# Performance work log

Measured on AMD Instinct MI355X. Metric: run time of the kernel, lower is better.

Reference implementation:

```python
import jax, jax.numpy as jnp
import numpy as np

NORMALIZED_LENGTH = 1.0
LOSS_WEIGHTS = (0.25, 1.0)
EPS = 1e-12  # matches torch F.normalize eps


def setup_inputs() -> dict:
    key = jax.random.key(0)
    k1, k2 = jax.random.split(key)
    x = jax.random.normal(k1, (16, 128, 64, 64), dtype=jnp.float32)
    codebook = jax.random.normal(k2, (1024, 128), dtype=jnp.float32)
    return {"x": x, "codebook": codebook}


def _forward(x, codebook):
    # --- VQCodebook.forward: normalize x along channel dim (dim=1) ---
    # NOTE: the torch source's codebook renormalization uses non-in-place
    # .div/.mul whose results are discarded, so the codebook is unchanged.
    if NORMALIZED_LENGTH > 0:
        nrm = jnp.linalg.norm(x, axis=1, keepdims=True)  # [B,1,H,W]
        x = NORMALIZED_LENGTH * x / jnp.maximum(nrm, EPS)

    B, C, H, W = x.shape
    z = jnp.transpose(x, (0, 2, 3, 1)).reshape(-1, C)  # [N, C], N = B*H*W

    # Pairwise squared L2 distances via ||z||^2 - 2 z c^T + ||c||^2.
    # argmin of squared distance == argmin of distance.
    z2 = jnp.sum(z * z, axis=1, keepdims=True)             # [N, 1]
    c2 = jnp.sum(codebook * codebook, axis=1)              # [K]
    d2 = z2 - 2.0 * jnp.einsum('nc,kc->nk', z, codebook) + c2[None, :]  # [N, K]
    idx = jnp.argmin(d2, axis=1)                           # [N]

    q = codebook[idx]                                      # [N, C]
    q = q.reshape(B, H, W, C).transpose(0, 3, 1, 2)        # [B, C, H, W]

    lw0, lw1 = LOSS_WEIGHTS
    diff_codebook = jax.lax.stop_gradient(x) - q
    diff_commit = x - jax.lax.stop_gradient(q)
    loss0 = lw0 * jnp.mean(jnp.linalg.norm(diff_codebook, axis=1))
    loss1 = lw1 * jnp.mean(jnp.linalg.norm(diff_commit, axis=1))
    return q, loss0, loss1


def reference(x, codebook):
    return _forward(x, codebook)
```

## Files before the change

kernel.cpp:

```cpp
#include <hip/hip_runtime.h>
#include <math.h>

#define K_CODES 1024
#define C_DIM   128
#define HW      4096
#define CHW     (C_DIM*HW)
#define N_POS   65536
#define Q_ELEMS 8388608

#define WS_S    0
#define WS_C2   256
#define WS_IDX  8192


typedef __attribute__((ext_vector_type(8))) short short8;
typedef __attribute__((ext_vector_type(4))) float f32x4;

__device__ __forceinline__ unsigned short f2bf(float f) {
    unsigned u = __float_as_uint(f);
    u += 0x7FFFu + ((u >> 16) & 1u);
    return (unsigned short)(u >> 16);
}

__device__ __forceinline__ void gll16(const void* g, void* l) {
    __builtin_amdgcn_global_load_lds(
        (const __attribute__((address_space(1))) void*)g,
        (__attribute__((address_space(3))) void*)l, 16, 0, 0);
}

__global__ void prep_kernel(const float* __restrict__ cb, float* __restrict__ ws,
                            unsigned short* __restrict__ cbbf) {
    __shared__ __align__(16) unsigned short srow[128];
    int k = blockIdx.x;
    int l = threadIdx.x;
    if (k == 0 && l == 0) *(float*)((char*)ws + WS_S) = 0.f;
    float v1 = cb[k * C_DIM + l];
    float v2 = cb[k * C_DIM + 64 + l];
    int c1 = l, c2 = 64 + l;
    srow[(((c1 >> 3) ^ (k & 7)) << 3) | (c1 & 7)] = f2bf(v1);
    srow[(((c2 >> 3) ^ (k & 7)) << 3) | (c2 & 7)] = f2bf(v2);
    float ss = v1 * v1 + v2 * v2;
    #pragma unroll
    for (int off = 32; off > 0; off >>= 1) ss += __shfl_down(ss, off);
    if (l == 0) ((float*)((char*)ws + WS_C2))[k] = ss;
    __syncthreads();
    if (l < 16) ((uint4*)cbbf)[k * 16 + l] = ((const uint4*)srow)[l];
}

__global__ __launch_bounds__(512, 2) void vq_mfma(const float* __restrict__ x,
                                                  const float* __restrict__ cb,
                                                  const unsigned short* __restrict__ cbbf,
                                                  const float* __restrict__ c2w,
                                                  int* __restrict__ idxw,
                                                  float* __restrict__ Sw) {
    __shared__ __align__(16) unsigned short cbuf[2][2 * 1024 * 8];
    __shared__ float mbuf[4][2][16][3];

    const int t  = threadIdx.x;
    const int w  = t >> 6;
    const int kh = w & 1;
    const int pg = w >> 1;
    const int ln = t & 63;
    const int lp = ln & 15;
    const int q  = ln >> 4;
    const int bid = blockIdx.x;
    const int b   = bid >> 5;
    const int s0  = (bid & 31) << 7;

    const char* gbase = (const char*)cbbf + kh * 131072 + pg * 4096 + ln * 16;
    const int   lofs  = kh * 16384 + pg * 4096;

    {
        char* l0 = (char*)cbuf[0] + lofs;
        #pragma unroll
        for (int r = 0; r < 4; ++r)
            gll16(gbase + r * 1024, l0 + r * 1024);
    }

    short8 xf[2][4];
    float  r2v[2];
    {
        float ss[2] = {0.f, 0.f};
        #pragma unroll
        for (int pt = 0; pt < 2; ++pt) {
            const float* xgp = x + b * CHW + s0 + pg * 32 + pt * 16 + lp;
            #pragma unroll
            for (int cs = 0; cs < 4; ++cs) {
                union { short8 v; unsigned short u[8]; } fu;
                #pragma unroll
                for (int j = 0; j < 8; ++j) {
                    float vv = xgp[(32 * cs + 8 * q + j) * HW];
                    ss[pt] = fmaf(vv, vv, ss[pt]);
                    fu.u[j] = f2bf(vv);
                }
                xf[pt][cs] = fu.v;
            }
        }
        #pragma unroll
        for (int pt = 0; pt < 2; ++pt) {
            float s = ss[pt];
            s += __shfl_xor(s, 16);
            s += __shfl_xor(s, 32);
            r2v[pt] = -2.0f / fmaxf(sqrtf(s), 1e-12f);
        }
    }

    const float FMAX = __uint_as_float(0x7F7FFFFFu);
    float m1[2] = {FMAX, FMAX}, m2[2] = {FMAX, FMAX}, m3[2] = {FMAX, FMAX};

    __syncthreads();

    for (int i = 0; i < 8; ++i) {
        if (i < 7) {
            char* ld = (char*)cbuf[(i + 1) & 1] + lofs;
            #pragma unroll
            for (int r = 0; r < 4; ++r)
                gll16(gbase + (i + 1) * 16384 + r * 1024, ld + r * 1024);
        }

        const int k0 = kh * 512 + i * 64;

        f32x4 acc[4][2];
        #pragma unroll
        for (int ct = 0; ct < 4; ++ct)
            #pragma unroll
            for (int pt = 0; pt < 2; ++pt) acc[ct][pt] = 0;

        const unsigned short* cbp = cbuf[i & 1] + kh * 8192;
        #pragma unroll
        for (int cs = 0; cs < 4; ++cs) {
            short8 ah[4];
            #pragma unroll
            for (int ct = 0; ct < 4; ++ct) {
                int g = (16 * ct + lp) * 16 + ((4 * cs + q) ^ (lp & 7));
                ah[ct] = *(const short8*)(cbp + g * 8);
            }
            #pragma unroll
            for (int ct = 0; ct < 4; ++ct)
                #pragma unroll
                for (int pt = 0; pt < 2; ++pt)
                    acc[ct][pt] = __builtin_amdgcn_mfma_f32_16x16x32_bf16(
                        ah[ct], xf[pt][cs], acc[ct][pt], 0, 0, 0);
        }

        #pragma unroll
        for (int ct = 0; ct < 4; ++ct) {
            float4 c2vv = *(const float4*)(c2w + k0 + 16 * ct + 4 * q);
            float c2a[4] = {c2vv.x, c2vv.y, c2vv.z, c2vv.w};
            const int kb0 = k0 + 16 * ct + 4 * q;
            #pragma unroll
            for (int pt = 0; pt < 2; ++pt) {
                #pragma unroll
                for (int reg = 0; reg < 4; ++reg) {
                    float s = fmaf(r2v[pt], acc[ct][pt][reg], c2a[reg]);
                    unsigned pb = (__float_as_uint(s) & 0xFFFFFC00u) |
                                  (unsigned)(kb0 + reg);
                    float u  = __uint_as_float(pb);
                    float t3 = __builtin_amdgcn_fmed3f(m2[pt], m3[pt], u);
                    float t2 = __builtin_amdgcn_fmed3f(m1[pt], m2[pt], u);
                    m1[pt] = fminf(m1[pt], u); m2[pt] = t2; m3[pt] = t3;
                }
            }
        }

        __syncthreads();
    }

    #pragma unroll
    for (int d = 16; d <= 32; d <<= 1) {
        #pragma unroll
        for (int pt = 0; pt < 2; ++pt) {
            float o1 = __shfl_xor(m1[pt], d), o2 = __shfl_xor(m2[pt], d),
                  o3 = __shfl_xor(m3[pt], d);
            float u, t2, t3;
            u = o1; t3 = __builtin_amdgcn_fmed3f(m2[pt], m3[pt], u);
            t2 = __builtin_amdgcn_fmed3f(m1[pt], m2[pt], u);
            m1[pt] = fminf(m1[pt], u); m2[pt] = t2; m3[pt] = t3;
            u = o2; t3 = __builtin_amdgcn_fmed3f(m2[pt], m3[pt], u);
            t2 = __builtin_amdgcn_fmed3f(m1[pt], m2[pt], u);
            m1[pt] = fminf(m1[pt], u); m2[pt] = t2; m3[pt] = t3;
            u = o3; t3 = __builtin_amdgcn_fmed3f(m2[pt], m3[pt], u);
            t2 = __builtin_amdgcn_fmed3f(m1[pt], m2[pt], u);
            m1[pt] = fminf(m1[pt], u); m2[pt] = t2; m3[pt] = t3;
        }
    }

    if (kh == 1 && ln < 16) {
        #pragma unroll
        for (int pt = 0; pt < 2; ++pt) {
            mbuf[pg][pt][lp][0] = m1[pt];
            mbuf[pg][pt][lp][1] = m2[pt];
            mbuf[pg][pt][lp][2] = m3[pt];
        }
    }
    __syncthreads();

    if (kh == 0) {
        float lsum = 0.f;
        #pragma unroll
        for (int pt = 0; pt < 2; ++pt) {
            #pragma unroll
            for (int c = 0; c < 3; ++c) {
                float u  = mbuf[pg][pt][lp][c];
                float t3 = __builtin_amdgcn_fmed3f(m2[pt], m3[pt], u);
                float t2 = __builtin_amdgcn_fmed3f(m1[pt], m2[pt], u);
                m1[pt] = fminf(m1[pt], u); m2[pt] = t2; m3[pt] = t3;
            }
            int ks[3] = {(int)(__float_as_uint(m1[pt]) & 1023u),
                         (int)(__float_as_uint(m2[pt]) & 1023u),
                         (int)(__float_as_uint(m3[pt]) & 1023u)};

            float xr[32];
            const float* xgp = x + b * CHW + s0 + pg * 32 + pt * 16 + lp;
            #pragma unroll
            for (int cs = 0; cs < 4; ++cs)
                #pragma unroll
                for (int j = 0; j < 8; ++j)
                    xr[cs * 8 + j] = xgp[(32 * cs + 8 * q + j) * HW];

            float dots[3];
            #pragma unroll
            for (int jj = 0; jj < 3; ++jj) {
                const float* crow = cb + ks[jj] * C_DIM + 8 * q;
                float p = 0.f;
                #pragma unroll
                for (int cs = 0; cs < 4; ++cs) {
                    float4 a0 = *(const float4*)(crow + 32 * cs);
                    float4 a1 = *(const float4*)(crow + 32 * cs + 4);
                    p = fmaf(xr[cs*8+0], a0.x, p); p = fmaf(xr[cs*8+1], a0.y, p);
                    p = fmaf(xr[cs*8+2], a0.z, p); p = fmaf(xr[cs*8+3], a0.w, p);
                    p = fmaf(xr[cs*8+4], a1.x, p); p = fmaf(xr[cs*8+5], a1.y, p);
                    p = fmaf(xr[cs*8+6], a1.z, p); p = fmaf(xr[cs*8+7], a1.w, p);
                }
                p += __shfl_xor(p, 16);
                p += __shfl_xor(p, 32);
                dots[jj] = p;
            }
            float sb = fmaf(r2v[pt], dots[0], c2w[ks[0]]); int kb = ks[0];
            float s2 = fmaf(r2v[pt], dots[1], c2w[ks[1]]);
            if (s2 < sb || (s2 == sb && ks[1] < kb)) { sb = s2; kb = ks[1]; }
            float s3 = fmaf(r2v[pt], dots[2], c2w[ks[2]]);
            if (s3 < sb || (s3 == sb && ks[2] < kb)) { sb = s3; kb = ks[2]; }

            if (ln < 16) idxw[bid * 128 + pg * 32 + pt * 16 + lp] = kb;
            lsum += sqrtf(fmaxf(1.0f + sb, 0.f));
        }
        #pragma unroll
        for (int off = 32; off > 0; off >>= 1) lsum += __shfl_down(lsum, off);
        if (ln == 0) atomicAdd(Sw, 0.25f * lsum);
    }
}

__global__ void write_q(const float* __restrict__ cb,
                        const int* __restrict__ idxw,
                        const float* __restrict__ ws,
                        float* __restrict__ out) {
    int id = blockIdx.x * 256 + threadIdx.x;
    int p  = id & (N_POS - 1);
    int c4 = id >> 16;
    int b  = p >> 12, s = p & 4095;
    int row = idxw[p];
    float4 v = ((const float4*)cb)[row * 32 + c4];
    float* o = out + b * CHW + (c4 * 4) * HW + s;
    o[0]      = v.x;
    o[HW]     = v.y;
    o[2 * HW] = v.z;
    o[3 * HW] = v.w;
    if (id == 0) {
        float S = *(const float*)((const char*)ws + WS_S);
        float m = S / (float)N_POS;
        out[Q_ELEMS]     = 0.25f * m;
        out[Q_ELEMS + 1] = m;
    }
}

extern "C" void kernel_launch(void* const* d_in, const int* in_sizes, int n_in,
                              void* d_out, int out_size, void* d_ws, size_t ws_size,
                              hipStream_t stream) {
    const float* x  = (const float*)d_in[0];
    const float* cb = (const float*)d_in[1];
    float* out = (float*)d_out;
    float* ws  = (float*)d_ws;

    const float* c2w = (const float*)((const char*)d_ws + WS_C2);
    int*  idxw = (int*)((char*)d_ws + WS_IDX);
    float* Sw  = (float*)((char*)d_ws + WS_S);
    unsigned short* cbbf = (unsigned short*)d_out;

    prep_kernel<<<K_CODES, 64, 0, stream>>>(cb, ws, cbbf);
    vq_mfma    <<<N_POS / 128, 512, 0, stream>>>(x, cb, cbbf, c2w, idxw, Sw);
    write_q    <<<Q_ELEMS / 1024, 256, 0, stream>>>(cb, idxw, ws, out);
}
```

Baseline: 78.11 us.

## Give each wave all 1024 codes and widen blocks to 256 positions

Result: slower. 99.76 us (+27.7%).

```diff
diff --git a/kernel.cpp b/kernel.cpp
--- a/kernel.cpp
+++ b/kernel.cpp
@@ -53,28 +53,24 @@
                                                   const float* __restrict__ c2w,
                                                   int* __restrict__ idxw,
                                                   float* __restrict__ Sw) {
-    __shared__ __align__(16) unsigned short cbuf[2][2 * 1024 * 8];
-    __shared__ float mbuf[4][2][16][3];
+    __shared__ __align__(16) unsigned short cbuf[2][32768];
 
     const int t  = threadIdx.x;
     const int w  = t >> 6;
-    const int kh = w & 1;
-    const int pg = w >> 1;
     const int ln = t & 63;
     const int lp = ln & 15;
     const int q  = ln >> 4;
     const int bid = blockIdx.x;
-    const int b   = bid >> 5;
-    const int s0  = (bid & 31) << 7;
-
-    const char* gbase = (const char*)cbbf + kh * 131072 + pg * 4096 + ln * 16;
-    const int   lofs  = kh * 16384 + pg * 4096;
+    const int b   = bid >> 4;
+    const int s0  = ((bid & 15) << 8) + (w << 5);
+
+    const char* gstage = (const char*)cbbf + (w << 13) + (ln << 4);
+    const int   lofs   = w << 13;
 
     {
         char* l0 = (char*)cbuf[0] + lofs;
         #pragma unroll
-        for (int r = 0; r < 4; ++r)
-            gll16(gbase + r * 1024, l0 + r * 1024);
+        for (int r = 0; r < 8; ++r) gll16(gstage + r * 1024, l0 + r * 1024);
     }
 
     short8 xf[2][4];
@@ -83,7 +79,7 @@
         float ss[2] = {0.f, 0.f};
         #pragma unroll
         for (int pt = 0; pt < 2; ++pt) {
-            const float* xgp = x + b * CHW + s0 + pg * 32 + pt * 16 + lp;
+            const float* xgp = x + b * CHW + s0 + pt * 16 + lp;
             #pragma unroll
             for (int cs = 0; cs < 4; ++cs) {
                 union { short8 v; unsigned short u[8]; } fu;
@@ -110,60 +106,65 @@
 
     __syncthreads();
 
-    for (int i = 0; i < 8; ++i) {
-        if (i < 7) {
-            char* ld = (char*)cbuf[(i + 1) & 1] + lofs;
-            #pragma unroll
-            for (int r = 0; r < 4; ++r)
-                gll16(gbase + (i + 1) * 16384 + r * 1024, ld + r * 1024);
-        }
-
-        const int k0 = kh * 512 + i * 64;
-
-        f32x4 acc[4][2];
-        #pragma unroll
-        for (int ct = 0; ct < 4; ++ct)
-            #pragma unroll
-            for (int pt = 0; pt < 2; ++pt) acc[ct][pt] = 0;
-
-        const unsigned short* cbp = cbuf[i & 1] + kh * 8192;
-        #pragma unroll
-        for (int cs = 0; cs < 4; ++cs) {
-            short8 ah[4];
+    for (int qt = 0; qt < 4; ++qt) {
+        if (qt < 3) {
+            char* ld = (char*)cbuf[(qt + 1) & 1] + lofs;
+            #pragma unroll
+            for (int r = 0; r < 8; ++r)
+                gll16(gstage + (qt + 1) * 65536 + r * 1024, ld + r * 1024);
+        }
+
+        const unsigned short* qbuf = cbuf[qt & 1];
+
+        #pragma unroll
+        for (int ic = 0; ic < 4; ++ic) {
+            const int k0 = (qt << 8) + (ic << 6);
+
+            f32x4 acc[4][2];
+            #pragma unroll
+            for (int ct = 0; ct < 4; ++ct)
+                #pragma unroll
+                for (int pt = 0; pt < 2; ++pt) acc[ct][pt] = 0;
+
+            const unsigned short* cbp = qbuf + ic * 8192;
+            #pragma unroll
+            for (int cs = 0; cs < 4; ++cs) {
+                short8 ah[4];
+                #pragma unroll
+                for (int ct = 0; ct < 4; ++ct) {
+                    int g = (16 * ct + lp) * 16 + ((4 * cs + q) ^ (lp & 7));
+                    ah[ct] = *(const short8*)(cbp + g * 8);
+                }
+                #pragma unroll
+                for (int ct = 0; ct < 4; ++ct)
+                    #pragma unroll
+                    for (int pt = 0; pt < 2; ++pt)
+                        acc[ct][pt] = __builtin_amdgcn_mfma_f32_16x16x32_bf16(
+                            ah[ct], xf[pt][cs], acc[ct][pt], 0, 0, 0);
+            }
+
             #pragma unroll
             for (int ct = 0; ct < 4; ++ct) {
-                int g = (16 * ct + lp) * 16 + ((4 * cs + q) ^ (lp & 7));
-                ah[ct] = *(const short8*)(cbp + g * 8);
-            }
-            #pragma unroll
-            for (int ct = 0; ct < 4; ++ct)
-                #pragma unroll
-                for (int pt = 0; pt < 2; ++pt)
-                    acc[ct][pt] = __builtin_amdgcn_mfma_f32_16x16x32_bf16(
-                        ah[ct], xf[pt][cs], acc[ct][pt], 0, 0, 0);
-        }
-
-        #pragma unroll
-        for (int ct = 0; ct < 4; ++ct) {
-            float4 c2vv = *(const float4*)(c2w + k0 + 16 * ct + 4 * q);
-            float c2a[4] = {c2vv.x, c2vv.y, c2vv.z, c2vv.w};
-            const int kb0 = k0 + 16 * ct + 4 * q;
-            #pragma unroll
-            for (int pt = 0; pt < 2; ++pt) {
-                #pragma unroll
-                for (int reg = 0; reg < 4; ++reg) {
-                    float s = fmaf(r2v[pt], acc[ct][pt][reg], c2a[reg]);
-                    unsigned pb = (__float_as_uint(s) & 0xFFFFFC00u) |
-                                  (unsigned)(kb0 + reg);
-                    float u  = __uint_as_float(pb);
-                    float t3 = __builtin_amdgcn_fmed3f(m2[pt], m3[pt], u);
-                    float t2 = __builtin_amdgcn_fmed3f(m1[pt], m2[pt], u);
-                    m1[pt] = fminf(m1[pt], u); m2[pt] = t2; m3[pt] = t3;
-                }
-            }
-        }
-
-        __syncthreads();
+                float4 c2vv = *(const float4*)(c2w + k0 + 16 * ct + 4 * q);
+                float c2a[4] = {c2vv.x, c2vv.y, c2vv.z, c2vv.w};
+                const int kb0 = k0 + 16 * ct + 4 * q;
+                #pragma unroll
+                for (int pt = 0; pt < 2; ++pt) {
+                    #pragma unroll
+                    for (int reg = 0; reg < 4; ++reg) {
+                        float s = fmaf(r2v[pt], acc[ct][pt][reg], c2a[reg]);
+                        unsigned pb = (__float_as_uint(s) & 0xFFFFFC00u) |
+                                      (unsigned)(kb0 + reg);
+                        float u  = __uint_as_float(pb);
+                        float t3 = __builtin_amdgcn_fmed3f(m2[pt], m3[pt], u);
+                        float t2 = __builtin_amdgcn_fmed3f(m1[pt], m2[pt], u);
+                        m1[pt] = fminf(m1[pt], u); m2[pt] = t2; m3[pt] = t3;
+                    }
+                }
+            }
+        }
+
+        if (qt < 3) __syncthreads();
     }
 
     #pragma unroll
@@ -185,33 +186,16 @@
         }
     }
 
-    if (kh == 1 && ln < 16) {
-        #pragma unroll
-        for (int pt = 0; pt < 2; ++pt) {
-            mbuf[pg][pt][lp][0] = m1[pt];
-            mbuf[pg][pt][lp][1] = m2[pt];
-            mbuf[pg][pt][lp][2] = m3[pt];
-        }
-    }
-    __syncthreads();
-
-    if (kh == 0) {
+    {
         float lsum = 0.f;
         #pragma unroll
         for (int pt = 0; pt < 2; ++pt) {
-            #pragma unroll
-            for (int c = 0; c < 3; ++c) {
-                float u  = mbuf[pg][pt][lp][c];
-                float t3 = __builtin_amdgcn_fmed3f(m2[pt], m3[pt], u);
-                float t2 = __builtin_amdgcn_fmed3f(m1[pt], m2[pt], u);
-                m1[pt] = fminf(m1[pt], u); m2[pt] = t2; m3[pt] = t3;
-            }
             int ks[3] = {(int)(__float_as_uint(m1[pt]) & 1023u),
                          (int)(__float_as_uint(m2[pt]) & 1023u),
                          (int)(__float_as_uint(m3[pt]) & 1023u)};
 
             float xr[32];
-            const float* xgp = x + b * CHW + s0 + pg * 32 + pt * 16 + lp;
+            const float* xgp = x + b * CHW + s0 + pt * 16 + lp;
             #pragma unroll
             for (int cs = 0; cs < 4; ++cs)
                 #pragma unroll
@@ -242,7 +226,7 @@
             float s3 = fmaf(r2v[pt], dots[2], c2w[ks[2]]);
             if (s3 < sb || (s3 == sb && ks[2] < kb)) { sb = s3; kb = ks[2]; }
 
-            if (ln < 16) idxw[bid * 128 + pg * 32 + pt * 16 + lp] = kb;
+            if (ln < 16) idxw[bid * 256 + (w << 5) + pt * 16 + lp] = kb;
             lsum += sqrtf(fmaxf(1.0f + sb, 0.f));
         }
         #pragma unroll
@@ -288,6 +272,6 @@
     unsigned short* cbbf = (unsigned short*)d_out;
 
     prep_kernel<<<K_CODES, 64, 0, stream>>>(cb, ws, cbbf);
-    vq_mfma    <<<N_POS / 128, 512, 0, stream>>>(x, cb, cbbf, c2w, idxw, Sw);
+    vq_mfma    <<<256, 512, 0, stream>>>(x, cb, cbbf, c2w, idxw, Sw);
     write_q    <<<Q_ELEMS / 1024, 256, 0, stream>>>(cb, idxw, ws, out);
 }
```
